# Kernel tuning notes

Hardware: AMD Instinct MI355X
Metric: run time of the kernel (lower is better)

## Reference

```python
import jax, jax.numpy as jnp
import numpy as np

# Config constants (match init_kwargs)
T = 1024            # num_tokens
H = 2048            # hidden_size
E = 16              # n_routed_experts
I = 1408            # moe_intermediate_size
TOP_K = 4           # num_experts_per_tok
N_GROUP = 4         # n_group
TOPK_GROUP = 2      # topk_group
N_SHARED = 2        # n_shared_experts
SI = I * N_SHARED   # shared intermediate = 2816
ROUTED_SCALE = 1.0  # routed_scaling_factor
RENORMALIZE = True  # norm_topk_prob


def setup_inputs() -> dict:
    key = jax.random.key(0)
    ks = jax.random.split(key, 6)
    scale_w = 0.02  # keep router logits in a sane range
    return {
        "x": jax.random.normal(ks[0], (T, H), dtype=jnp.float32),
        "gate_w": jax.random.normal(ks[1], (E, H), dtype=jnp.float32) * scale_w,
        "w_gate_up": jax.random.normal(ks[2], (E, H, 2 * I), dtype=jnp.float32) * scale_w,
        "w_down": jax.random.normal(ks[3], (E, I, H), dtype=jnp.float32) * scale_w,
        "shared_gate_up": jax.random.normal(ks[4], (H, 2 * SI), dtype=jnp.float32) * scale_w,
        "shared_down": jax.random.normal(ks[5], (SI, H), dtype=jnp.float32) * scale_w,
    }


def _silu_and_mul(gu):
    gate, up = jnp.split(gu, 2, axis=-1)
    return jax.nn.silu(gate) * up


def _grouped_topk(logits):
    # scores over experts, grouped top-k group selection, then top-k experts
    scores = jax.nn.softmax(logits, axis=-1)                          # [T, E]
    group_scores = scores.reshape(T, N_GROUP, E // N_GROUP).max(-1)   # [T, G]
    _, grp_idx = jax.lax.top_k(group_scores, TOPK_GROUP)              # [T, topk_group]
    grp_mask = jnp.zeros((T, N_GROUP), scores.dtype).at[
        jnp.arange(T)[:, None], grp_idx].set(1.0)                     # [T, G]
    score_mask = jnp.repeat(grp_mask, E // N_GROUP, axis=1)           # [T, E]
    tmp = jnp.where(score_mask > 0, scores, 0.0)
    topk_w, topk_ids = jax.lax.top_k(tmp, TOP_K)                      # [T, K]
    if RENORMALIZE:
        topk_w = topk_w / jnp.sum(topk_w, axis=-1, keepdims=True)
    # dense combine-weight matrix [T, E] (top-k ids are distinct per token)
    cw = jnp.zeros((T, E), scores.dtype).at[
        jnp.arange(T)[:, None], topk_ids].set(topk_w)
    return cw


def reference(x, gate_w, w_gate_up, w_down, shared_gate_up, shared_down):
    # shared experts MLP (SiluAndMul)
    shared_out = _silu_and_mul(x @ shared_gate_up) @ shared_down      # [T, H]

    # router
    logits = x @ gate_w.T                                             # [T, E]
    cw = _grouped_topk(logits)                                        # [T, E]

    # routed experts: dense grouped GEMM over all experts, masked combine
    h = jnp.einsum('th,ehi->eti', x, w_gate_up)                       # [E, T, 2I]
    a = _silu_and_mul(h)                                              # [E, T, I]
    y = jnp.einsum('eti,eih->eth', a, w_down)                         # [E, T, H]
    routed = jnp.einsum('eth,te->th', y, cw)                          # [T, H]

    return routed * ROUTED_SCALE + shared_out
```

## Files before the change

### kernel.cpp

```cpp
#include <hip/hip_runtime.h>
#include <hip/hip_bf16.h>
#include <stdint.h>
#include <math.h>

#define T_TOK 1024
#define H_DIM 2048
#define E_NUM 16
#define I_DIM 1408
#define TOPK  4
#define SI_DIM 2816
#define NSLOT (T_TOK * TOPK)

typedef short bf16x8 __attribute__((ext_vector_type(8)));
typedef float f32x4  __attribute__((ext_vector_type(4)));

__device__ __forceinline__ uint32_t fbf(float f) {
  __hip_bfloat16 h = __float2bfloat16(f);
  return (uint32_t)*reinterpret_cast<uint16_t*>(&h);
}
__device__ __forceinline__ float asf(uint32_t u) {
  union { uint32_t u; float f; } c; c.u = u; return c.f;
}

typedef const __attribute__((address_space(1))) char gld_g;
typedef __attribute__((address_space(3))) char gld_l;
__device__ __forceinline__ void gload16(const void* g, void* l) {
  __builtin_amdgcn_global_load_lds((gld_g*)g, (gld_l*)l, 16, 0, 0);
}
__device__ __forceinline__ void barrier_lgkm() {
  asm volatile("s_waitcnt lgkmcnt(0)" ::: "memory");
  __builtin_amdgcn_s_barrier();
  __builtin_amdgcn_sched_barrier(0);
}

__global__ __launch_bounds__(256) void k_router(const float* __restrict__ x,
                                                const float* __restrict__ gw,
                                                int* __restrict__ topk_id,
                                                float* __restrict__ topk_w) {
  int t = blockIdx.x;
  float acc[E_NUM];
#pragma unroll
  for (int e = 0; e < E_NUM; ++e) acc[e] = 0.f;
  for (int h = threadIdx.x; h < H_DIM; h += 256) {
    float xv = x[(long)t * H_DIM + h];
#pragma unroll
    for (int e = 0; e < E_NUM; ++e) acc[e] += xv * gw[e * H_DIM + h];
  }
#pragma unroll
  for (int e = 0; e < E_NUM; ++e) {
#pragma unroll
    for (int off = 32; off; off >>= 1) acc[e] += __shfl_down(acc[e], off);
  }
  __shared__ float part[4][E_NUM];
  int wid = threadIdx.x >> 6, lane = threadIdx.x & 63;
  if (lane == 0) {
#pragma unroll
    for (int e = 0; e < E_NUM; ++e) part[wid][e] = acc[e];
  }
  __syncthreads();
  if (threadIdx.x == 0) {
    float lg[E_NUM], p[E_NUM];
    float m = -1e30f;
    for (int e = 0; e < E_NUM; ++e) {
      lg[e] = part[0][e] + part[1][e] + part[2][e] + part[3][e];
      m = fmaxf(m, lg[e]);
    }
    float s = 0.f;
    for (int e = 0; e < E_NUM; ++e) { p[e] = expf(lg[e] - m); s += p[e]; }
    float inv = 1.f / s;
    for (int e = 0; e < E_NUM; ++e) p[e] *= inv;
    float gs[4];
    for (int g = 0; g < 4; ++g) {
      float mg = p[g * 4];
      for (int i = 1; i < 4; ++i) mg = fmaxf(mg, p[g * 4 + i]);
      gs[g] = mg;
    }
    int g1 = 0;
    for (int g = 1; g < 4; ++g) if (gs[g] > gs[g1]) g1 = g;
    int g2 = -1;
    for (int g = 0; g < 4; ++g) {
      if (g == g1) continue;
      if (g2 < 0 || gs[g] > gs[g2]) g2 = g;
    }
    float q[E_NUM];
    for (int e = 0; e < E_NUM; ++e)
      q[e] = ((e >> 2) == g1 || (e >> 2) == g2) ? p[e] : -1e30f;
    int ids[TOPK]; float wv[TOPK]; float wsum = 0.f;
    for (int k = 0; k < TOPK; ++k) {
      int best = 0; float bv = -2e30f;
      for (int e = 0; e < E_NUM; ++e) if (q[e] > bv) { bv = q[e]; best = e; }
      ids[k] = best; wv[k] = p[best]; wsum += p[best]; q[best] = -3e30f;
    }
    float winv = 1.f / wsum;
    for (int k = 0; k < TOPK; ++k) {
      topk_id[t * TOPK + k] = ids[k];
      topk_w[t * TOPK + k] = wv[k] * winv;
    }
  }
}

__global__ __launch_bounds__(256) void k_count(const int* __restrict__ topk_id,
                                               int* __restrict__ counts) {
  int e = blockIdx.x, tid = threadIdx.x;
  int c = 0;
  for (int s = tid; s < NSLOT; s += 256) c += (topk_id[s] == e);
#pragma unroll
  for (int off = 32; off; off >>= 1) c += __shfl_down(c, off);
  __shared__ int wsum[4];
  int wid = tid >> 6, lane = tid & 63;
  if (lane == 0) wsum[wid] = c;
  __syncthreads();
  if (tid == 0) counts[e] = wsum[0] + wsum[1] + wsum[2] + wsum[3];
}

__global__ void k_offs(const int* __restrict__ counts, int* __restrict__ offs,
                       int* __restrict__ cum) {
  if (threadIdx.x == 0 && blockIdx.x == 0) {
    int s = 0, c = 0;
    cum[0] = 0;
    for (int e = 0; e < E_NUM; ++e) {
      offs[e] = s; s += counts[e];
      c += (counts[e] + 127) >> 7;
      cum[e + 1] = c;
    }
    offs[E_NUM] = s;
  }
}

__global__ __launch_bounds__(256) void k_fill(const int* __restrict__ topk_id,
                                              const int* __restrict__ offs,
                                              int* __restrict__ tok_of_row,
                                              int* __restrict__ row_of_slot) {
  int e = blockIdx.x, tid = threadIdx.x;
  int t0 = tid * 4;
  int match[4]; int cnt = 0;
#pragma unroll
  for (int i = 0; i < 4; ++i) {
    int t = t0 + i; int mk = -1;
#pragma unroll
    for (int k = 0; k < TOPK; ++k) if (topk_id[t * TOPK + k] == e) mk = k;
    match[i] = mk; cnt += (mk >= 0);
  }
  __shared__ int sc[256];
  sc[tid] = cnt; __syncthreads();
  for (int d = 1; d < 256; d <<= 1) {
    int v = sc[tid];
    if (tid >= d) v += sc[tid - d];
    __syncthreads();
    sc[tid] = v;
    __syncthreads();
  }
  int row = offs[e] + sc[tid] - cnt;
#pragma unroll
  for (int i = 0; i < 4; ++i) {
    if (match[i] >= 0) {
      tok_of_row[row] = t0 + i;
      row_of_slot[(t0 + i) * TOPK + match[i]] = row;
      ++row;
    }
  }
}

__global__ __launch_bounds__(256) void k_cvt(const float* __restrict__ in,
                                             uint16_t* __restrict__ out) {
  int i = (blockIdx.x * 256 + threadIdx.x) * 4;
  float4 v = *(const float4*)(in + i);
  uint2 p;
  p.x = fbf(v.x) | (fbf(v.y) << 16);
  p.y = fbf(v.z) | (fbf(v.w) << 16);
  *(uint2*)(out + i) = p;
}

template <int MODE>
__global__ __launch_bounds__(256, 4) void k_gemm(
    const uint16_t* __restrict__ As, int ldas,
    const float* __restrict__ Bs, int ldbs, int upS,
    void* __restrict__ OutS, int ldoS, int NMs, int NNs, int Ks, int f32S,
    const uint16_t* __restrict__ Ar, int ldar,
    const float* __restrict__ Br, int ldbr, long bstr, int upR,
    void* __restrict__ OutR, int ldoR, int NN1, int K1, int f32R,
    const int* __restrict__ offs, const int* __restrict__ rowlist,
    const int* __restrict__ cum) {
  constexpr int BN = (MODE == 0) ? 64 : 128;
  constexpr int NI = (MODE == 0) ? 2 : 4;
  constexpr int BB = 16384;
  constexpr int BMS = 5120;
  __shared__ char smem[26624];

  const int S = NMs * NNs;
  const int NBw = S + cum[E_NUM] * NN1;
  int f = blockIdx.x;
  if (f >= NBw) return;
  int q = NBw >> 3, r = NBw & 7;
  int xcd = f & 7, o = f >> 3;
  int f2 = (xcd < r ? xcd * (q + 1) : r * (q + 1) + (xcd - r) * q) + o;

  const uint16_t* A; const float* Bp; void* Outp; const int* rl;
  int lda, ldb, up, ldo, K, m0, n0, row_end, isf32;
  if (f2 < S) {
    int mb = f2 % NMs, nb = f2 / NMs;
    A = As; lda = ldas; Bp = Bs; ldb = ldbs; up = upS;
    Outp = OutS; ldo = ldoS; K = Ks; isf32 = f32S; rl = nullptr;
    m0 = mb * 128; row_end = NMs * 128; n0 = nb * BN;
  } else {
    int g = f2 - S;
    int e = 0;
    for (e = 0; e < E_NUM; ++e) if (g < cum[e + 1] * NN1) break;
    int nmbe = cum[e + 1] - cum[e];
    int loc = g - cum[e] * NN1;
    int mb = loc % nmbe, nb = loc / nmbe;
    A = Ar; lda = ldar; Bp = Br + (size_t)e * bstr; ldb = ldbr; up = upR;
    Outp = OutR; ldo = ldoR; K = K1; isf32 = f32R; rl = rowlist;
    m0 = offs[e] + mb * 128; row_end = offs[e + 1]; n0 = nb * BN;
  }

  const int tid = threadIdx.x;
  const int wid = tid >> 6, lane = tid & 63;
  const int wm = (wid >> 1) * 64, wn = (wid & 1) * (BN / 2);
  const int lrow = lane & 15, kg = lane >> 4;

  const uint16_t* aSrc[2]; int aDst[2];
#pragma unroll
  for (int p = 0; p < 2; ++p) {
    int rr = wid * 32 + p * 16 + (lane >> 2);
    int grow = m0 + rr;
    grow = grow < row_end - 1 ? grow : row_end - 1;
    int arow = rl ? rl[grow] : grow;
    aSrc[p] = A + (size_t)arow * lda + (lane & 3) * 8;
    aDst[p] = wid * 2048 + p * 1024;
  }

  int n4, kq, mat;
  if constexpr (MODE == 0) {
    n4 = (tid & 15) * 4; int rest = tid >> 4; kq = rest & 7; mat = rest >> 3;
  } else {
    n4 = (tid & 31) * 4; kq = tid >> 5; mat = 0;
  }
  const int k0 = kq * 4;
  const float* bptr = Bp + (size_t)k0 * ldb + n0 + n4 + (mat ? up : 0);
  const int sq = (kq >> 1) & 3, hf = kq & 1;
  int bw[4];
#pragma unroll
  for (int j = 0; j < 4; ++j) {
    int n = n4 + j;
    bw[j] = BB + mat * BMS + n * 80 + ((sq ^ ((n >> 4) & 3)) << 4) + (hf << 3);
  }

  float4 v[4];
  auto loadB = [&]() {
#pragma unroll
    for (int i = 0; i < 4; ++i) v[i] = *(const float4*)(bptr + (size_t)i * ldb);
    bptr += (size_t)32 * ldb;
  };
  auto stageB = [&]() {
#pragma unroll
    for (int j = 0; j < 4; ++j) {
      uint2 w;
      w.x = fbf(((const float*)&v[0])[j]) | (fbf(((const float*)&v[1])[j]) << 16);
      w.y = fbf(((const float*)&v[2])[j]) | (fbf(((const float*)&v[3])[j]) << 16);
      *(uint2*)(smem + bw[j]) = w;
    }
  };

  f32x4 zero = {0.f, 0.f, 0.f, 0.f};
  f32x4 accg[4][NI];
  f32x4 accu[(MODE == 0) ? 4 : 1][(MODE == 0) ? NI : 1];
#pragma unroll
  for (int mi = 0; mi < 4; ++mi)
#pragma unroll
    for (int ni = 0; ni < NI; ++ni) {
      accg[mi][ni] = zero;
      if constexpr (MODE == 0) accu[mi][ni] = zero;
    }

  const int nk = K >> 5;
#pragma unroll
  for (int p = 0; p < 2; ++p) { gload16(aSrc[p], smem + aDst[p]); aSrc[p] += 32; }
  loadB();

  for (int kt = 0; kt < nk; ++kt) {
    const int cur = kt & 1;
    __syncthreads();
    if (kt + 1 < nk) {
#pragma unroll
      for (int p = 0; p < 2; ++p) {
        gload16(aSrc[p], smem + (cur ^ 1) * 8192 + aDst[p]); aSrc[p] += 32;
      }
    }
    stageB();
    if (kt + 1 < nk) loadB();
    barrier_lgkm();

    const char* abuf = smem + cur * 8192;
    bf16x8 af[4];
#pragma unroll
    for (int mi = 0; mi < 4; ++mi)
      af[mi] = *(const bf16x8*)(abuf + (wm + mi * 16 + lrow) * 64 + kg * 16);
#pragma unroll
    for (int ni = 0; ni < NI; ++ni) {
      int n = wn + ni * 16 + lrow;
      int bo = BB + n * 80 + ((kg ^ ((n >> 4) & 3)) << 4);
      bf16x8 bg = *(const bf16x8*)(smem + bo);
#pragma unroll
      for (int mi = 0; mi < 4; ++mi)
        accg[mi][ni] = __builtin_amdgcn_mfma_f32_16x16x32_bf16(
            af[mi], bg, accg[mi][ni], 0, 0, 0);
      if constexpr (MODE == 0) {
        bf16x8 bu = *(const bf16x8*)(smem + bo + BMS);
#pragma unroll
        for (int mi = 0; mi < 4; ++mi)
          accu[mi][ni] = __builtin_amdgcn_mfma_f32_16x16x32_bf16(
              af[mi], bu, accu[mi][ni], 0, 0, 0);
      }
    }
  }

#pragma unroll
  for (int mi = 0; mi < 4; ++mi) {
#pragma unroll
    for (int rr = 0; rr < 4; ++rr) {
      int grow = m0 + wm + mi * 16 + kg * 4 + rr;
      if (grow >= row_end) continue;
#pragma unroll
      for (int ni = 0; ni < NI; ++ni) {
        int col = n0 + wn + ni * 16 + lrow;
        float g = accg[mi][ni][rr];
        if constexpr (MODE == 0) {
          float u = accu[mi][ni][rr];
          float a = g / (1.f + __expf(-g)) * u;
          ((uint16_t*)Outp)[(size_t)grow * ldo + col] = (uint16_t)fbf(a);
        } else {
          if (isf32)
            ((float*)Outp)[(size_t)grow * ldo + col] = g;
          else
            ((uint16_t*)Outp)[(size_t)grow * ldo + col] = (uint16_t)fbf(g);
        }
      }
    }
  }
}

__global__ __launch_bounds__(256) void k_combine(float* __restrict__ out,
    const uint16_t* __restrict__ y, const int* __restrict__ row_of_slot,
    const float* __restrict__ topk_w, const float* __restrict__ p0) {
  int t = blockIdx.x, tid = threadIdx.x;
  int h = tid * 8;
  size_t off = (size_t)t * H_DIM + h;
  float4 o0 = *(const float4*)(p0 + off);
  float4 o1 = *(const float4*)(p0 + off + 4);
#pragma unroll
  for (int k = 0; k < TOPK; ++k) {
    int row = row_of_slot[t * TOPK + k];
    float wk = topk_w[t * TOPK + k];
    uint4 v = *(const uint4*)(y + (size_t)row * H_DIM + h);
    o0.x += wk * asf(v.x << 16); o0.y += wk * asf(v.x & 0xffff0000u);
    o0.z += wk * asf(v.y << 16); o0.w += wk * asf(v.y & 0xffff0000u);
    o1.x += wk * asf(v.z << 16); o1.y += wk * asf(v.z & 0xffff0000u);
    o1.z += wk * asf(v.w << 16); o1.w += wk * asf(v.w & 0xffff0000u);
  }
  *(float4*)(out + off) = o0;
  *(float4*)(out + off + 4) = o1;
}

extern "C" void kernel_launch(void* const* d_in, const int* in_sizes, int n_in,
                              void* d_out, int out_size, void* d_ws,
                              size_t ws_size, hipStream_t stream) {
  const float* x   = (const float*)d_in[0];
  const float* gw  = (const float*)d_in[1];
  const float* wgu = (const float*)d_in[2];
  const float* wd  = (const float*)d_in[3];
  const float* sgu = (const float*)d_in[4];
  const float* sd  = (const float*)d_in[5];
  float* out = (float*)d_out;

  char* ws = (char*)d_ws;
  int*   topk_id     = (int*)(ws + 0);
  float* topk_w      = (float*)(ws + 16384);
  int*   counts      = (int*)(ws + 32768);
  int*   offs        = (int*)(ws + 33792);
  int*   cum         = (int*)(ws + 34816);
  int*   tok_of_row  = (int*)(ws + 35840);
  int*   row_of_slot = (int*)(ws + 52224);
  uint16_t* x_bf     = (uint16_t*)(ws + 131072);
  uint16_t* act      = (uint16_t*)(ws + 4325376);
  uint16_t* yslots   = (uint16_t*)(ws + 15859712);
  uint16_t* act_sh   = (uint16_t*)(ws + 32636928);
  bool merged = ws_size >= (size_t)38404096 + 8388608;
  float* p0 = merged ? (float*)(ws + 38404096) : (float*)(ws + 4325376);

  k_router<<<T_TOK, 256, 0, stream>>>(x, gw, topk_id, topk_w);
  k_count<<<E_NUM, 256, 0, stream>>>(topk_id, counts);
  k_offs<<<1, 1, 0, stream>>>(counts, offs, cum);
  k_fill<<<E_NUM, 256, 0, stream>>>(topk_id, offs, tok_of_row, row_of_slot);
  k_cvt<<<(T_TOK * H_DIM) / 1024, 256, 0, stream>>>(x, x_bf);

  k_gemm<0><<<352 + 48 * 22, 256, 0, stream>>>(
      x_bf, H_DIM, sgu, 2 * SI_DIM, SI_DIM, act_sh, SI_DIM, 8, 44, H_DIM, 0,
      x_bf, H_DIM, wgu, 2 * I_DIM, (long)H_DIM * 2 * I_DIM, I_DIM,
      act, I_DIM, 22, H_DIM, 0,
      offs, tok_of_row, cum);

  if (merged) {
    k_gemm<1><<<128 + 48 * 16, 256, 0, stream>>>(
        act_sh, SI_DIM, sd, H_DIM, 0, p0, H_DIM, 8, 16, SI_DIM, 1,
        act, I_DIM, wd, H_DIM, (long)I_DIM * H_DIM, 0,
        yslots, H_DIM, 16, I_DIM, 0,
        offs, nullptr, cum);
  } else {
    k_gemm<1><<<48 * 16, 256, 0, stream>>>(
        act_sh, SI_DIM, sd, H_DIM, 0, p0, H_DIM, 8, 0, SI_DIM, 1,
        act, I_DIM, wd, H_DIM, (long)I_DIM * H_DIM, 0,
        yslots, H_DIM, 16, I_DIM, 0,
        offs, nullptr, cum);
    k_gemm<1><<<128, 256, 0, stream>>>(
        act_sh, SI_DIM, sd, H_DIM, 0, p0, H_DIM, 8, 16, SI_DIM, 1,
        act, I_DIM, wd, H_DIM, (long)I_DIM * H_DIM, 0,
        yslots, H_DIM, 0, I_DIM, 0,
        offs, nullptr, cum);
  }
  k_combine<<<T_TOK, 256, 0, stream>>>(out, yslots, row_of_slot, topk_w, p0);
}
```

Before: 348.9 us.

## Enlarge GEMM tiles to 256-row blocks with 512 threads and BK=64

The grouped and shared GEMM kernel moves from 128-row, 256-thread tiles with a 32-wide K step to 256-row tiles run by 512 threads, doubles the output tile width, and uses a 64-wide K step. This cuts the number of blocks and the number of loop iterations with their barriers. The A tile in LDS gets an XOR swizzle and the B tile a padded layout. The pipeline uses explicit vmcnt waits, scheduling barriers and priority bumps. Expert blocks are now rounded to 256 rows, so experts with few tokens waste more MFMA work, and the roughly 100 KB of LDS per block limits occupancy and tail balance.

```diff
diff --git a/kernel.cpp b/kernel.cpp
--- a/kernel.cpp
+++ b/kernel.cpp
@@ -120,7 +120,7 @@
     cum[0] = 0;
     for (int e = 0; e < E_NUM; ++e) {
       offs[e] = s; s += counts[e];
-      c += (counts[e] + 127) >> 7;
+      c += (counts[e] + 255) >> 8;
       cum[e + 1] = c;
     }
     offs[E_NUM] = s;
@@ -172,7 +172,7 @@
 }
 
 template <int MODE>
-__global__ __launch_bounds__(256, 4) void k_gemm(
+__global__ __launch_bounds__(512, 2) void k_gemm(
     const uint16_t* __restrict__ As, int ldas,
     const float* __restrict__ Bs, int ldbs, int upS,
     void* __restrict__ OutS, int ldoS, int NMs, int NNs, int Ks, int f32S,
@@ -181,11 +181,11 @@
     void* __restrict__ OutR, int ldoR, int NN1, int K1, int f32R,
     const int* __restrict__ offs, const int* __restrict__ rowlist,
     const int* __restrict__ cum) {
-  constexpr int BN = (MODE == 0) ? 64 : 128;
+  constexpr int BNOUT = (MODE == 0) ? 128 : 256;
   constexpr int NI = (MODE == 0) ? 2 : 4;
-  constexpr int BB = 16384;
-  constexpr int BMS = 5120;
-  __shared__ char smem[26624];
+  constexpr int BB = 65536;
+  constexpr int BMS = 18432;
+  __shared__ char smem[102400];
 
   const int S = NMs * NNs;
   const int NBw = S + cum[E_NUM] * NN1;
@@ -201,122 +201,141 @@
     int mb = f2 % NMs, nb = f2 / NMs;
     A = As; lda = ldas; Bp = Bs; ldb = ldbs; up = upS;
     Outp = OutS; ldo = ldoS; K = Ks; isf32 = f32S; rl = nullptr;
-    m0 = mb * 128; row_end = NMs * 128; n0 = nb * BN;
+    m0 = mb * 256; row_end = NMs * 256; n0 = nb * BNOUT;
   } else {
     int g = f2 - S;
     int e = 0;
     for (e = 0; e < E_NUM; ++e) if (g < cum[e + 1] * NN1) break;
+    if (e == E_NUM) return;
     int nmbe = cum[e + 1] - cum[e];
     int loc = g - cum[e] * NN1;
     int mb = loc % nmbe, nb = loc / nmbe;
     A = Ar; lda = ldar; Bp = Br + (size_t)e * bstr; ldb = ldbr; up = upR;
     Outp = OutR; ldo = ldoR; K = K1; isf32 = f32R; rl = rowlist;
-    m0 = offs[e] + mb * 128; row_end = offs[e + 1]; n0 = nb * BN;
+    m0 = offs[e] + mb * 256; row_end = offs[e + 1]; n0 = nb * BNOUT;
   }
 
   const int tid = threadIdx.x;
   const int wid = tid >> 6, lane = tid & 63;
-  const int wm = (wid >> 1) * 64, wn = (wid & 1) * (BN / 2);
+  const int wm = (wid >> 2) * 128;
+  const int wn = (wid & 3) * ((MODE == 0) ? 32 : 64);
   const int lrow = lane & 15, kg = lane >> 4;
 
-  const uint16_t* aSrc[2]; int aDst[2];
-#pragma unroll
-  for (int p = 0; p < 2; ++p) {
-    int rr = wid * 32 + p * 16 + (lane >> 2);
+  const uint16_t* aSrc[4]; int aDst[4];
+#pragma unroll
+  for (int p = 0; p < 4; ++p) {
+    int rr = p * 64 + wid * 8 + (lane >> 3);
     int grow = m0 + rr;
     grow = grow < row_end - 1 ? grow : row_end - 1;
     int arow = rl ? rl[grow] : grow;
-    aSrc[p] = A + (size_t)arow * lda + (lane & 3) * 8;
-    aDst[p] = wid * 2048 + p * 1024;
-  }
-
-  int n4, kq, mat;
+    aSrc[p] = A + (size_t)arow * lda + (((lane & 7) ^ ((lane >> 3) & 7)) << 3);
+    aDst[p] = p * 8192 + wid * 1024;
+  }
+  auto issueA = [&](int buf) {
+#pragma unroll
+    for (int p = 0; p < 4; ++p) {
+      gload16(aSrc[p], smem + buf * 32768 + aDst[p]);
+      aSrc[p] += 64;
+    }
+  };
+
+  int mat, kq, nq;
   if constexpr (MODE == 0) {
-    n4 = (tid & 15) * 4; int rest = tid >> 4; kq = rest & 7; mat = rest >> 3;
+    mat = tid >> 8; kq = tid & 7; nq = (tid >> 3) & 31;
   } else {
-    n4 = (tid & 31) * 4; kq = tid >> 5; mat = 0;
-  }
-  const int k0 = kq * 4;
-  const float* bptr = Bp + (size_t)k0 * ldb + n0 + n4 + (mat ? up : 0);
-  const int sq = (kq >> 1) & 3, hf = kq & 1;
-  int bw[4];
-#pragma unroll
-  for (int j = 0; j < 4; ++j) {
-    int n = n4 + j;
-    bw[j] = BB + mat * BMS + n * 80 + ((sq ^ ((n >> 4) & 3)) << 4) + (hf << 3);
-  }
-
-  float4 v[4];
-  auto loadB = [&]() {
-#pragma unroll
-    for (int i = 0; i < 4; ++i) v[i] = *(const float4*)(bptr + (size_t)i * ldb);
-    bptr += (size_t)32 * ldb;
+    mat = 0; kq = tid & 7; nq = tid >> 3;
+  }
+  const float* bptr = Bp + (size_t)(kq * 8) * ldb + n0 + nq * 4 + (mat ? up : 0);
+  int bwOff[4];
+#pragma unroll
+  for (int j = 0; j < 4; ++j)
+    bwOff[j] = BB + mat * BMS + (nq * 4 + j) * 144 + kq * 16;
+
+  float4 bv[8];
+  auto issueB = [&]() {
+#pragma unroll
+    for (int jj = 0; jj < 8; ++jj)
+      bv[jj] = *(const float4*)(bptr + (size_t)jj * ldb);
+    bptr += (size_t)64 * ldb;
   };
-  auto stageB = [&]() {
+  auto writeB = [&]() {
 #pragma unroll
     for (int j = 0; j < 4; ++j) {
-      uint2 w;
-      w.x = fbf(((const float*)&v[0])[j]) | (fbf(((const float*)&v[1])[j]) << 16);
-      w.y = fbf(((const float*)&v[2])[j]) | (fbf(((const float*)&v[3])[j]) << 16);
-      *(uint2*)(smem + bw[j]) = w;
+      uint4 w;
+      w.x = fbf(((const float*)&bv[0])[j]) | (fbf(((const float*)&bv[1])[j]) << 16);
+      w.y = fbf(((const float*)&bv[2])[j]) | (fbf(((const float*)&bv[3])[j]) << 16);
+      w.z = fbf(((const float*)&bv[4])[j]) | (fbf(((const float*)&bv[5])[j]) << 16);
+      w.w = fbf(((const float*)&bv[6])[j]) | (fbf(((const float*)&bv[7])[j]) << 16);
+      *(uint4*)(smem + bwOff[j]) = w;
     }
   };
 
   f32x4 zero = {0.f, 0.f, 0.f, 0.f};
-  f32x4 accg[4][NI];
-  f32x4 accu[(MODE == 0) ? 4 : 1][(MODE == 0) ? NI : 1];
-#pragma unroll
-  for (int mi = 0; mi < 4; ++mi)
+  f32x4 accg[8][NI];
+  f32x4 accu[(MODE == 0) ? 8 : 1][(MODE == 0) ? NI : 1];
+#pragma unroll
+  for (int mi = 0; mi < 8; ++mi)
 #pragma unroll
     for (int ni = 0; ni < NI; ++ni) {
       accg[mi][ni] = zero;
       if constexpr (MODE == 0) accu[mi][ni] = zero;
     }
 
-  const int nk = K >> 5;
-#pragma unroll
-  for (int p = 0; p < 2; ++p) { gload16(aSrc[p], smem + aDst[p]); aSrc[p] += 32; }
-  loadB();
-
-  for (int kt = 0; kt < nk; ++kt) {
-    const int cur = kt & 1;
-    __syncthreads();
-    if (kt + 1 < nk) {
-#pragma unroll
-      for (int p = 0; p < 2; ++p) {
-        gload16(aSrc[p], smem + (cur ^ 1) * 8192 + aDst[p]); aSrc[p] += 32;
+  auto compute = [&](int buf) {
+    const char* ab = smem + buf * 32768;
+#pragma unroll
+    for (int ks = 0; ks < 2; ++ks) {
+      const int sk = (ks << 2) | kg;
+      bf16x8 af[8];
+#pragma unroll
+      for (int mi = 0; mi < 8; ++mi) {
+        int row = wm + mi * 16 + lrow;
+        af[mi] = *(const bf16x8*)(ab + row * 128 + ((sk ^ (lrow & 7)) << 4));
       }
-    }
-    stageB();
-    if (kt + 1 < nk) loadB();
+#pragma unroll
+      for (int ni = 0; ni < NI; ++ni) {
+        int n = wn + ni * 16 + lrow;
+        bf16x8 bg = *(const bf16x8*)(smem + BB + n * 144 + sk * 16);
+#pragma unroll
+        for (int mi = 0; mi < 8; ++mi)
+          accg[mi][ni] = __builtin_amdgcn_mfma_f32_16x16x32_bf16(
+              af[mi], bg, accg[mi][ni], 0, 0, 0);
+        if constexpr (MODE == 0) {
+          bf16x8 bu = *(const bf16x8*)(smem + BB + BMS + n * 144 + sk * 16);
+#pragma unroll
+          for (int mi = 0; mi < 8; ++mi)
+            accu[mi][ni] = __builtin_amdgcn_mfma_f32_16x16x32_bf16(
+                af[mi], bu, accu[mi][ni], 0, 0, 0);
+        }
+      }
+    }
+  };
+
+  const int nt = K >> 6;
+  issueA(0);
+  issueB();
+
+  for (int t = 0; t < nt; ++t) {
+    if (t + 1 < nt) {
+      issueA((t + 1) & 1);
+      asm volatile("s_waitcnt vmcnt(4)" ::: "memory");
+    } else {
+      asm volatile("s_waitcnt vmcnt(0)" ::: "memory");
+    }
+    __builtin_amdgcn_sched_barrier(0);
+    writeB();
+    if (t + 1 < nt) issueB();
+    asm volatile("s_waitcnt lgkmcnt(0)" ::: "memory");
+    __builtin_amdgcn_s_barrier();
+    __builtin_amdgcn_sched_barrier(0);
+    __builtin_amdgcn_s_setprio(1);
+    compute(t & 1);
+    __builtin_amdgcn_s_setprio(0);
     barrier_lgkm();
-
-    const char* abuf = smem + cur * 8192;
-    bf16x8 af[4];
-#pragma unroll
-    for (int mi = 0; mi < 4; ++mi)
-      af[mi] = *(const bf16x8*)(abuf + (wm + mi * 16 + lrow) * 64 + kg * 16);
-#pragma unroll
-    for (int ni = 0; ni < NI; ++ni) {
-      int n = wn + ni * 16 + lrow;
-      int bo = BB + n * 80 + ((kg ^ ((n >> 4) & 3)) << 4);
-      bf16x8 bg = *(const bf16x8*)(smem + bo);
-#pragma unroll
-      for (int mi = 0; mi < 4; ++mi)
-        accg[mi][ni] = __builtin_amdgcn_mfma_f32_16x16x32_bf16(
-            af[mi], bg, accg[mi][ni], 0, 0, 0);
-      if constexpr (MODE == 0) {
-        bf16x8 bu = *(const bf16x8*)(smem + bo + BMS);
-#pragma unroll
-        for (int mi = 0; mi < 4; ++mi)
-          accu[mi][ni] = __builtin_amdgcn_mfma_f32_16x16x32_bf16(
-              af[mi], bu, accu[mi][ni], 0, 0, 0);
-      }
-    }
-  }
-
-#pragma unroll
-  for (int mi = 0; mi < 4; ++mi) {
+  }
+
+#pragma unroll
+  for (int mi = 0; mi < 8; ++mi) {
 #pragma unroll
     for (int rr = 0; rr < 4; ++rr) {
       int grow = m0 + wm + mi * 16 + kg * 4 + rr;
@@ -394,26 +413,26 @@
   k_fill<<<E_NUM, 256, 0, stream>>>(topk_id, offs, tok_of_row, row_of_slot);
   k_cvt<<<(T_TOK * H_DIM) / 1024, 256, 0, stream>>>(x, x_bf);
 
-  k_gemm<0><<<352 + 48 * 22, 256, 0, stream>>>(
-      x_bf, H_DIM, sgu, 2 * SI_DIM, SI_DIM, act_sh, SI_DIM, 8, 44, H_DIM, 0,
+  k_gemm<0><<<88 + 32 * 11, 512, 0, stream>>>(
+      x_bf, H_DIM, sgu, 2 * SI_DIM, SI_DIM, act_sh, SI_DIM, 4, 22, H_DIM, 0,
       x_bf, H_DIM, wgu, 2 * I_DIM, (long)H_DIM * 2 * I_DIM, I_DIM,
-      act, I_DIM, 22, H_DIM, 0,
+      act, I_DIM, 11, H_DIM, 0,
       offs, tok_of_row, cum);
 
   if (merged) {
-    k_gemm<1><<<128 + 48 * 16, 256, 0, stream>>>(
-        act_sh, SI_DIM, sd, H_DIM, 0, p0, H_DIM, 8, 16, SI_DIM, 1,
+    k_gemm<1><<<32 + 32 * 8, 512, 0, stream>>>(
+        act_sh, SI_DIM, sd, H_DIM, 0, p0, H_DIM, 4, 8, SI_DIM, 1,
         act, I_DIM, wd, H_DIM, (long)I_DIM * H_DIM, 0,
-        yslots, H_DIM, 16, I_DIM, 0,
+        yslots, H_DIM, 8, I_DIM, 0,
         offs, nullptr, cum);
   } else {
-    k_gemm<1><<<48 * 16, 256, 0, stream>>>(
-        act_sh, SI_DIM, sd, H_DIM, 0, p0, H_DIM, 8, 0, SI_DIM, 1,
+    k_gemm<1><<<32 * 8, 512, 0, stream>>>(
+        act_sh, SI_DIM, sd, H_DIM, 0, p0, H_DIM, 4, 0, SI_DIM, 1,
         act, I_DIM, wd, H_DIM, (long)I_DIM * H_DIM, 0,
-        yslots, H_DIM, 16, I_DIM, 0,
+        yslots, H_DIM, 8, I_DIM, 0,
         offs, nullptr, cum);
-    k_gemm<1><<<128, 256, 0, stream>>>(
-        act_sh, SI_DIM, sd, H_DIM, 0, p0, H_DIM, 8, 16, SI_DIM, 1,
+    k_gemm<1><<<32, 512, 0, stream>>>(
+        act_sh, SI_DIM, sd, H_DIM, 0, p0, H_DIM, 4, 8, SI_DIM, 1,
         act, I_DIM, wd, H_DIM, (long)I_DIM * H_DIM, 0,
         yslots, H_DIM, 0, I_DIM, 0,
         offs, nullptr, cum);
```

Result: slower. 383.9 us (+10.0%).
